# Optimization experiments

Measured on AMD Instinct MI355X. Metric: run time of the kernel, lower is better.

Reference implementation:

```python
import jax, jax.numpy as jnp
import numpy as np

N = 100000   # num_nodes
E = 300000   # num directed edges (symmetrized to 2E inside forward)
D = 128      # input_dim
O = 128      # output_dim
R = 32       # num_relations
B = 8        # num_bases


def setup_inputs() -> dict:
    key = jax.random.key(0)
    ks = jax.random.split(key, 8)
    x = jax.random.normal(ks[0], (N, D), dtype=jnp.float32)
    node_keep_mask = jax.random.randint(ks[1], (N,), 0, 2) > 0
    source = jax.random.randint(ks[2], (E,), 0, N, dtype=jnp.int32)
    target = jax.random.randint(ks[3], (E,), 0, N, dtype=jnp.int32)
    edge_type = jax.random.randint(ks[4], (E,), 0, R, dtype=jnp.int32)
    edge_weights = jax.random.uniform(ks[5], (E,), dtype=jnp.float32)
    # xavier_normal for bases
    std = (2.0 / (D + O)) ** 0.5
    bases = jax.random.normal(ks[6], (B, D, O), dtype=jnp.float32) * std
    # uniform then L1-normalized rows, shape (R+1, B); row R is the self-loop
    rbw = jax.random.uniform(ks[7], (R + 1, B), dtype=jnp.float32)
    rbw = rbw / jnp.sum(rbw, axis=1, keepdims=True)
    return {
        "x": x,
        "node_keep_mask": node_keep_mask,
        "source": source,
        "target": target,
        "edge_type": edge_type,
        "edge_weights": edge_weights,
        "bases": bases,
        "relation_base_weights": rbw,
    }


def reference(x, node_keep_mask, source, target, edge_type, edge_weights,
              bases, relation_base_weights):
    # Self-loop: weight for relation id == num_relations (last row)
    w_self = jnp.einsum("bij,b->ij", bases, relation_base_weights[-1])
    out = jnp.where(node_keep_mask[:, None], x @ w_self, jnp.zeros((), x.dtype))

    # Symmetrize edges: messages flow in both directions (same relation/weight)
    src = jnp.concatenate([source, target])          # (2E,)
    tgt = jnp.concatenate([target, source])          # (2E,)
    etype = jnp.concatenate([edge_type, edge_type])  # (2E,)
    ew = jnp.concatenate([edge_weights, edge_weights])  # (2E,)

    # Project all nodes through every basis once: (N, B, O)
    proj = jnp.einsum("nd,bdo->nbo", x, bases)
    # Per-edge basis coefficients from the edge's relation: (2E, B)
    coeff = relation_base_weights[etype]
    # Message: x[src] @ (sum_b coeff_b * base_b) == sum_b coeff_b * proj[src, b]
    msg = jnp.einsum("eb,ebo->eo", coeff, proj[src])  # (2E, O)
    msg = msg * ew[:, None]

    # Scatter-add messages into target nodes
    out = out.at[tgt].add(msg)
    return out
```

## Files before the change

### kernel.cpp

```cpp
#include <hip/hip_runtime.h>

typedef __attribute__((ext_vector_type(8))) __bf16 bf16x8;
typedef __attribute__((ext_vector_type(4))) float f32x4;
typedef __attribute__((ext_vector_type(2))) float f32x2;
typedef __attribute__((ext_vector_type(8))) unsigned short ushortx8;

__device__ inline unsigned short f2bf(float f) {
  unsigned int u = __float_as_uint(f);
  unsigned int r = (u + 0x7FFFu + ((u >> 16) & 1u)) >> 16;
  return (unsigned short)r;
}

__global__ __launch_bounds__(256) void prep_kernel(const float* __restrict__ x,
                                                   unsigned short* __restrict__ xb, int total8,
                                                   const float* __restrict__ bases,
                                                   unsigned short* __restrict__ bmt,
                                                   const int* __restrict__ src,
                                                   const int* __restrict__ tgt, int E,
                                                   int* __restrict__ cnt,
                                                   const unsigned char* __restrict__ mask,
                                                   int mbytes, int* __restrict__ flag_out,
                                                   int CB, int TB, int HB) {
  int bid = blockIdx.x;
  if (bid < CB) {
    int id = bid * 256 + threadIdx.x;
    if (id >= total8) return;
    f32x4 f0 = ((const f32x4*)x)[2 * id];
    f32x4 f1 = ((const f32x4*)x)[2 * id + 1];
    ushortx8 r;
    r[0] = f2bf(f0[0]); r[1] = f2bf(f0[1]); r[2] = f2bf(f0[2]); r[3] = f2bf(f0[3]);
    r[4] = f2bf(f1[0]); r[5] = f2bf(f1[1]); r[6] = f2bf(f1[2]); r[7] = f2bf(f1[3]);
    ((ushortx8*)xb)[id] = r;
  } else if (bid < CB + TB) {
    int id = (bid - CB) * 256 + threadIdx.x;
    if (id >= 128 * 1024) return;
    int o = id >> 10, k = id & 1023, b = k >> 7, d = k & 127;
    bmt[id] = f2bf(bases[b * 16384 + d * 128 + o]);
  } else if (bid < CB + TB + HB) {
    int i = (bid - CB - TB) * 256 + threadIdx.x;
    if (i >= E) return;
    atomicAdd(&cnt[tgt[i]], 1);
    atomicAdd(&cnt[src[i]], 1);
  } else {
    __shared__ int nz_off, big;
    if (threadIdx.x == 0) { nz_off = 0; big = 0; }
    __syncthreads();
    int lnz = 0, lbig = 0;
    for (int i = threadIdx.x; i < mbytes; i += 256) {
      unsigned char v = mask[i];
      if ((i & 3) && v) lnz++;
      if (v > 1) lbig++;
    }
    if (lnz) atomicAdd(&nz_off, lnz);
    if (lbig) atomicAdd(&big, lbig);
    __syncthreads();
    if (threadIdx.x == 0) *flag_out = (nz_off == 0) ? 0 : ((big == 0) ? 1 : 2);
  }
}

__global__ __launch_bounds__(256) void scan1_kernel(const int* __restrict__ cnt, int N,
                                                    int* __restrict__ bsum) {
  __shared__ int s[256];
  int t = threadIdx.x, i = blockIdx.x * 256 + t;
  s[t] = (i < N) ? cnt[i] : 0;
  __syncthreads();
#pragma unroll
  for (int off = 128; off > 0; off >>= 1) {
    if (t < off) s[t] += s[t + off];
    __syncthreads();
  }
  if (t == 0) bsum[blockIdx.x] = s[0];
}

__global__ void scan2_kernel(const int* __restrict__ bsum, int nb,
                             int* __restrict__ bexcl, int* __restrict__ base, int N) {
  __shared__ int s[512];
  int t = threadIdx.x;
  int v = (t < nb) ? bsum[t] : 0;
  s[t] = v;
  __syncthreads();
  for (int off = 1; off < 512; off <<= 1) {
    int x = (t >= off) ? s[t - off] : 0;
    __syncthreads();
    s[t] += x;
    __syncthreads();
  }
  if (t < nb) bexcl[t] = s[t] - v;
  if (t == nb - 1) base[N] = s[t];
}

__global__ __launch_bounds__(256) void scan3_kernel(const int* __restrict__ cnt, int N,
                                                    const int* __restrict__ bexcl,
                                                    int* __restrict__ base,
                                                    int* __restrict__ cursor) {
  __shared__ int s[256];
  int t = threadIdx.x, i = blockIdx.x * 256 + t;
  int c = (i < N) ? cnt[i] : 0;
  s[t] = c;
  __syncthreads();
  for (int off = 1; off < 256; off <<= 1) {
    int x = (t >= off) ? s[t - off] : 0;
    __syncthreads();
    s[t] += x;
    __syncthreads();
  }
  if (i < N) {
    int v = bexcl[blockIdx.x] + s[t] - c;
    base[i] = v;
    cursor[i] = v;
  }
}

__global__ __launch_bounds__(256) void scatter_kernel(const int* __restrict__ src,
                                                      const int* __restrict__ tgt,
                                                      const int* __restrict__ et,
                                                      const float* __restrict__ ew, int E,
                                                      const float* __restrict__ rbw,
                                                      int* __restrict__ cursor,
                                                      unsigned* __restrict__ msrc,
                                                      uint4* __restrict__ mcoef) {
  __shared__ float ctab[264];
  for (int i = threadIdx.x; i < 264; i += 256) ctab[i] = rbw[i];
  __syncthreads();
  int i = blockIdx.x * 256 + threadIdx.x;
  if (i >= E) return;
  int s = src[i], g = tgt[i], r = et[i];
  float w = ew[i];
  uint4 cv;
  {
    const float* c = &ctab[r * 8];
    cv.x = (unsigned)f2bf(w * c[0]) | ((unsigned)f2bf(w * c[1]) << 16);
    cv.y = (unsigned)f2bf(w * c[2]) | ((unsigned)f2bf(w * c[3]) << 16);
    cv.z = (unsigned)f2bf(w * c[4]) | ((unsigned)f2bf(w * c[5]) << 16);
    cv.w = (unsigned)f2bf(w * c[6]) | ((unsigned)f2bf(w * c[7]) << 16);
  }
  int s1 = atomicAdd(&cursor[g], 1);
  msrc[s1] = (unsigned)s;
  mcoef[s1] = cv;
  int s2 = atomicAdd(&cursor[s], 1);
  msrc[s2] = (unsigned)g;
  mcoef[s2] = cv;
}

__global__ void pad_kernel(unsigned* __restrict__ msrc, uint4* __restrict__ mcoef, int M) {
  int t = threadIdx.x;
  if (t < 8) {
    msrc[M + t] = 0u;
    mcoef[M + t] = make_uint4(0u, 0u, 0u, 0u);
  }
}

__global__ __launch_bounds__(512, 4) void gather_kernel(
    const unsigned* __restrict__ xb32, const unsigned short* __restrict__ bmt,
    const int* __restrict__ base, const unsigned* __restrict__ msrc,
    const uint4* __restrict__ mcoef, const float* __restrict__ rbw,
    const void* __restrict__ maskp, const int* __restrict__ flag_p,
    float* __restrict__ out, int N) {
  extern __shared__ char smem[];
  int t = threadIdx.x;
  int wid = t >> 6, l = t & 63;
  int t0 = blockIdx.x * 32;
  int flag = *flag_p;

  for (int j = 0; j < 4; ++j) {
    int tg = __builtin_amdgcn_readfirstlane(t0 + wid * 4 + j);
    int tgc = min(tg, N - 1);
    int beg = __builtin_amdgcn_readfirstlane(base[tgc]);
    int cnt = __builtin_amdgcn_readfirstlane(base[tgc + 1]) - beg;
    if (tg >= N) cnt = 0;
    unsigned xs = xb32[(size_t)tgc * 64 + l];
    int keep;
    if (flag == 0)      keep = ((const int*)maskp)[tgc] != 0;
    else if (flag == 1) keep = ((const unsigned char*)maskp)[tgc] != 0;
    else                keep = ((const float*)maskp)[tgc] != 0.f;
    float ms = (keep && tg < N) ? 1.f : 0.f;
    f32x2 xv0 = {__uint_as_float(xs << 16), __uint_as_float(xs & 0xFFFF0000u)};
    f32x2 z[8];
#pragma unroll
    for (int b = 0; b < 8; ++b) {
      float a = ms * rbw[256 + b];
      z[b] = (f32x2){a, a} * xv0;
    }
    for (int mb = 0; mb < cnt; mb += 8) {
      unsigned rowv[8];
      uint4 cf[8];
#pragma unroll
      for (int s = 0; s < 8; ++s) {
        rowv[s] = msrc[beg + mb + s];
        cf[s] = mcoef[beg + mb + s];
      }
      unsigned xr[8];
#pragma unroll
      for (int s = 0; s < 8; ++s) xr[s] = xb32[(size_t)rowv[s] * 64 + l];
#pragma unroll
      for (int s = 0; s < 8; ++s) {
        unsigned vm = ((mb + s) < cnt) ? 0xFFFFFFFFu : 0u;
        f32x2 xv = {__uint_as_float(xr[s] << 16), __uint_as_float(xr[s] & 0xFFFF0000u)};
        unsigned cw[4] = {cf[s].x & vm, cf[s].y & vm, cf[s].z & vm, cf[s].w & vm};
#pragma unroll
        for (int q = 0; q < 4; ++q) {
          float a0 = __uint_as_float(cw[q] << 16);
          float a1 = __uint_as_float(cw[q] & 0xFFFF0000u);
          z[2 * q] = __builtin_elementwise_fma((f32x2){a0, a0}, xv, z[2 * q]);
          z[2 * q + 1] = __builtin_elementwise_fma((f32x2){a1, a1}, xv, z[2 * q + 1]);
        }
      }
    }
    int row = wid * 4 + j;
#pragma unroll
    for (int b = 0; b < 8; ++b) {
      unsigned pk = (unsigned)f2bf(z[b][0]) | ((unsigned)f2bf(z[b][1]) << 16);
      int byte = row * 2048 + ((b * 256 + l * 4) ^ ((row & 7) << 4));
      *(unsigned*)(smem + byte) = pk;
    }
  }
  __syncthreads();

  int l15 = l & 15, lk8 = (l >> 4) * 8;
  f32x4 acc[2] = {};
  for (int ks = 0; ks < 32; ++ks) {
    int k0 = ks * 32 + lk8;
    bf16x8 a[2], bb;
#pragma unroll
    for (int rt = 0; rt < 2; ++rt) {
      int tr = rt * 16 + l15;
      int byte = tr * 2048 + ((k0 * 2) ^ ((tr & 7) << 4));
      a[rt] = *(const bf16x8*)(smem + byte);
    }
    int col = wid * 16 + l15;
    bb = *(const bf16x8*)(bmt + (size_t)col * 1024 + k0);
#pragma unroll
    for (int rt = 0; rt < 2; ++rt)
      acc[rt] = __builtin_amdgcn_mfma_f32_16x16x32_bf16(a[rt], bb, acc[rt], 0, 0, 0);
  }
#pragma unroll
  for (int rt = 0; rt < 2; ++rt) {
    int rowb = t0 + rt * 16 + (l >> 4) * 4;
    int col = wid * 16 + l15;
#pragma unroll
    for (int i = 0; i < 4; ++i) {
      int row = rowb + i;
      if (row < N) out[(size_t)row * 128 + col] = acc[rt][i];
    }
  }
}

extern "C" void kernel_launch(void* const* d_in, const int* in_sizes, int n_in,
                              void* d_out, int out_size, void* d_ws, size_t ws_size,
                              hipStream_t stream) {
  const float* x = (const float*)d_in[0];
  const void* mask = d_in[1];
  const int* source = (const int*)d_in[2];
  const int* target = (const int*)d_in[3];
  const int* etype = (const int*)d_in[4];
  const float* eweight = (const float*)d_in[5];
  const float* bases = (const float*)d_in[6];
  const float* rbw = (const float*)d_in[7];
  float* out = (float*)d_out;

  const int N = in_sizes[1];
  const int E = in_sizes[2];
  const int M = 2 * E;
  const int NB = (N + 255) / 256;

  char* ws = (char*)d_ws;
  size_t off = 0;
  unsigned short* xb = (unsigned short*)(ws + off); off += (size_t)N * 256;
  unsigned short* bmt = (unsigned short*)(ws + off); off += 128 * 1024 * 2;
  unsigned* msrc = (unsigned*)(ws + off); off += (size_t)(M + 16) * 4;
  uint4* mcoef = (uint4*)(ws + off); off += (size_t)(M + 16) * 16;
  int* base = (int*)(ws + off); off += ((size_t)N + 64) * 4;
  int* cursor = (int*)(ws + off); off += ((size_t)N + 64) * 4;
  int* cnt = (int*)(ws + off); off += ((size_t)N + 64) * 4;
  int* bsum = (int*)(ws + off); off += 2048;
  int* bexcl = (int*)(ws + off); off += 2048;
  int* flag = (int*)(ws + off); off += 256;

  hipMemsetAsync(cnt, 0, (size_t)N * 4, stream);
  int total8 = (N * 128) / 8;
  int CB = (total8 + 255) / 256;
  int TB = (128 * 1024 + 255) / 256;
  int HB = (E + 255) / 256;
  prep_kernel<<<CB + TB + HB + 1, 256, 0, stream>>>(x, xb, total8, bases, bmt,
                                                    source, target, E, cnt,
                                                    (const unsigned char*)mask,
                                                    N < 8192 ? N : 8192, flag, CB, TB, HB);
  scan1_kernel<<<NB, 256, 0, stream>>>(cnt, N, bsum);
  scan2_kernel<<<1, 512, 0, stream>>>(bsum, NB, bexcl, base, N);
  scan3_kernel<<<NB, 256, 0, stream>>>(cnt, N, bexcl, base, cursor);
  scatter_kernel<<<(E + 255) / 256, 256, 0, stream>>>(source, target, etype, eweight, E,
                                                      rbw, cursor, msrc, mcoef);
  pad_kernel<<<1, 64, 0, stream>>>(msrc, mcoef, M);
  int gblk = (N + 31) / 32;
  size_t shmem = 65536;
  gather_kernel<<<gblk, 512, shmem, stream>>>((const unsigned*)xb, bmt, base, msrc, mcoef,
                                              rbw, mask, flag, out, N);
}
```

Measured before the change: 249.9 us.

## Stage block edge lists in LDS and software-pipeline paired node gathers

The gather kernel now copies each block's message-source indices and coefficients into shared memory when they fit (up to MC entries), then processes two target nodes per wave at once. Row loads for the next group of four messages are double-buffered ahead of the FMAs on the current group, so more gather loads are in flight. This aims to hide gather latency and avoid repeated global index loads, at the cost of more LDS (which may reduce occupancy below 4 blocks per CU) and more registers, plus an extra sync.

```diff
diff --git a/kernel.cpp b/kernel.cpp
--- a/kernel.cpp
+++ b/kernel.cpp
@@ -4,6 +4,8 @@
 typedef __attribute__((ext_vector_type(4))) float f32x4;
 typedef __attribute__((ext_vector_type(2))) float f32x2;
 typedef __attribute__((ext_vector_type(8))) unsigned short ushortx8;
+
+#define MC 384
 
 __device__ inline unsigned short f2bf(float f) {
   unsigned int u = __float_as_uint(f);
@@ -150,6 +152,79 @@
   }
 }
 
+template <bool LDSM>
+__device__ __forceinline__ void load_quad(const unsigned* __restrict__ xb32,
+                                          const unsigned* lms,
+                                          const unsigned* __restrict__ gms, int B0,
+                                          int loc, int mb, int cnt, int l,
+                                          unsigned (&xr)[4]) {
+  if (mb < cnt) {
+#pragma unroll
+    for (int s = 0; s < 4; ++s) {
+      int lo = loc + mb + s;
+      unsigned row = LDSM ? lms[lo] : gms[B0 + lo];
+      xr[s] = xb32[(size_t)row * 64 + l];
+    }
+  }
+}
+
+template <bool LDSM>
+__device__ __forceinline__ void fma_quad(const uint4* lmc,
+                                         const uint4* __restrict__ gmc, int B0,
+                                         int loc, int mb, int cnt,
+                                         const unsigned (&xr)[4], f32x2 (&z)[8]) {
+  if (mb < cnt) {
+#pragma unroll
+    for (int s = 0; s < 4; ++s) {
+      int lo = loc + mb + s;
+      uint4 cf = LDSM ? lmc[lo] : gmc[B0 + lo];
+      unsigned vm = ((mb + s) < cnt) ? 0xFFFFFFFFu : 0u;
+      f32x2 xv = {__uint_as_float(xr[s] << 16), __uint_as_float(xr[s] & 0xFFFF0000u)};
+      unsigned c0 = cf.x & vm, c1 = cf.y & vm, c2 = cf.z & vm, c3 = cf.w & vm;
+      float a;
+      a = __uint_as_float(c0 << 16);          z[0] = __builtin_elementwise_fma((f32x2){a, a}, xv, z[0]);
+      a = __uint_as_float(c0 & 0xFFFF0000u);  z[1] = __builtin_elementwise_fma((f32x2){a, a}, xv, z[1]);
+      a = __uint_as_float(c1 << 16);          z[2] = __builtin_elementwise_fma((f32x2){a, a}, xv, z[2]);
+      a = __uint_as_float(c1 & 0xFFFF0000u);  z[3] = __builtin_elementwise_fma((f32x2){a, a}, xv, z[3]);
+      a = __uint_as_float(c2 << 16);          z[4] = __builtin_elementwise_fma((f32x2){a, a}, xv, z[4]);
+      a = __uint_as_float(c2 & 0xFFFF0000u);  z[5] = __builtin_elementwise_fma((f32x2){a, a}, xv, z[5]);
+      a = __uint_as_float(c3 << 16);          z[6] = __builtin_elementwise_fma((f32x2){a, a}, xv, z[6]);
+      a = __uint_as_float(c3 & 0xFFFF0000u);  z[7] = __builtin_elementwise_fma((f32x2){a, a}, xv, z[7]);
+    }
+  }
+}
+
+template <bool LDSM>
+__device__ __forceinline__ void do_pair(const unsigned* __restrict__ xb32,
+                                        const unsigned* lms, const uint4* lmc,
+                                        const unsigned* __restrict__ gms,
+                                        const uint4* __restrict__ gmc, int B0,
+                                        int locA, int cntA, int locB, int cntB, int l,
+                                        f32x2 (&zA)[8], f32x2 (&zB)[8]) {
+  int rounds = (max(cntA, cntB) + 3) >> 2;
+  if (rounds <= 0) return;
+  unsigned xA0[4], xA1[4], xB0[4], xB1[4];
+  load_quad<LDSM>(xb32, lms, gms, B0, locA, 0, cntA, l, xA0);
+  load_quad<LDSM>(xb32, lms, gms, B0, locB, 0, cntB, l, xB0);
+  int r = 0;
+  while (true) {
+    if (r + 1 < rounds) {
+      load_quad<LDSM>(xb32, lms, gms, B0, locA, (r + 1) * 4, cntA, l, xA1);
+      load_quad<LDSM>(xb32, lms, gms, B0, locB, (r + 1) * 4, cntB, l, xB1);
+    }
+    fma_quad<LDSM>(lmc, gmc, B0, locA, r * 4, cntA, xA0, zA);
+    fma_quad<LDSM>(lmc, gmc, B0, locB, r * 4, cntB, xB0, zB);
+    if (++r >= rounds) break;
+    if (r + 1 < rounds) {
+      load_quad<LDSM>(xb32, lms, gms, B0, locA, (r + 1) * 4, cntA, l, xA0);
+      load_quad<LDSM>(xb32, lms, gms, B0, locB, (r + 1) * 4, cntB, l, xB0);
+    }
+    fma_quad<LDSM>(lmc, gmc, B0, locA, r * 4, cntA, xA1, zA);
+    fma_quad<LDSM>(lmc, gmc, B0, locB, r * 4, cntB, xB1, zB);
+    if (++r >= rounds) break;
+  }
+}
+
 __global__ __launch_bounds__(512, 4) void gather_kernel(
     const unsigned* __restrict__ xb32, const unsigned short* __restrict__ bmt,
     const int* __restrict__ base, const unsigned* __restrict__ msrc,
@@ -157,61 +232,75 @@
     const void* __restrict__ maskp, const int* __restrict__ flag_p,
     float* __restrict__ out, int N) {
   extern __shared__ char smem[];
+  unsigned* lms = (unsigned*)(smem + 65536);
+  uint4* lmc = (uint4*)(smem + 65536 + 1536);
+  int* lbase = (int*)(smem + 65536 + 1536 + 6144);
   int t = threadIdx.x;
   int wid = t >> 6, l = t & 63;
   int t0 = blockIdx.x * 32;
   int flag = *flag_p;
 
-  for (int j = 0; j < 4; ++j) {
-    int tg = __builtin_amdgcn_readfirstlane(t0 + wid * 4 + j);
-    int tgc = min(tg, N - 1);
-    int beg = __builtin_amdgcn_readfirstlane(base[tgc]);
-    int cnt = __builtin_amdgcn_readfirstlane(base[tgc + 1]) - beg;
-    if (tg >= N) cnt = 0;
-    unsigned xs = xb32[(size_t)tgc * 64 + l];
-    int keep;
-    if (flag == 0)      keep = ((const int*)maskp)[tgc] != 0;
-    else if (flag == 1) keep = ((const unsigned char*)maskp)[tgc] != 0;
-    else                keep = ((const float*)maskp)[tgc] != 0.f;
-    float ms = (keep && tg < N) ? 1.f : 0.f;
-    f32x2 xv0 = {__uint_as_float(xs << 16), __uint_as_float(xs & 0xFFFF0000u)};
-    f32x2 z[8];
+  if (t < 33) lbase[t] = base[min(t0 + t, N)];
+  int B0 = __builtin_amdgcn_readfirstlane(base[min(t0, N)]);
+  int B1 = __builtin_amdgcn_readfirstlane(base[min(t0 + 32, N)]);
+  int nm = B1 - B0;
+  bool use_lds = (nm <= MC);
+  if (use_lds) {
+    for (int i = t; i < nm; i += 512) {
+      lms[i] = msrc[B0 + i];
+      lmc[i] = mcoef[B0 + i];
+    }
+    if (t < 8 && nm + t < MC) {
+      lms[nm + t] = 0u;
+      lmc[nm + t] = make_uint4(0u, 0u, 0u, 0u);
+    }
+  }
+  __syncthreads();
+
+  for (int p = 0; p < 2; ++p) {
+    int jA = wid * 4 + p * 2, jB = jA + 1;
+    int tgA = t0 + jA, tgB = t0 + jB;
+    int tcA = min(tgA, N - 1), tcB = min(tgB, N - 1);
+    int begA = __builtin_amdgcn_readfirstlane(lbase[jA]);
+    int begB = __builtin_amdgcn_readfirstlane(lbase[jB]);
+    int endB = __builtin_amdgcn_readfirstlane(lbase[jB + 1]);
+    int cntA = (tgA < N) ? (begB - begA) : 0;
+    int cntB = (tgB < N) ? (endB - begB) : 0;
+    int locA = begA - B0, locB = begB - B0;
+    unsigned xsA = xb32[(size_t)tcA * 64 + l];
+    unsigned xsB = xb32[(size_t)tcB * 64 + l];
+    int keepA, keepB;
+    if (flag == 0) {
+      keepA = ((const int*)maskp)[tcA] != 0; keepB = ((const int*)maskp)[tcB] != 0;
+    } else if (flag == 1) {
+      keepA = ((const unsigned char*)maskp)[tcA] != 0; keepB = ((const unsigned char*)maskp)[tcB] != 0;
+    } else {
+      keepA = ((const float*)maskp)[tcA] != 0.f; keepB = ((const float*)maskp)[tcB] != 0.f;
+    }
+    float msA = (keepA && tgA < N) ? 1.f : 0.f;
+    float msB = (keepB && tgB < N) ? 1.f : 0.f;
+    f32x2 zA[8], zB[8];
+    f32x2 xvA = {__uint_as_float(xsA << 16), __uint_as_float(xsA & 0xFFFF0000u)};
+    f32x2 xvB = {__uint_as_float(xsB << 16), __uint_as_float(xsB & 0xFFFF0000u)};
 #pragma unroll
     for (int b = 0; b < 8; ++b) {
-      float a = ms * rbw[256 + b];
-      z[b] = (f32x2){a, a} * xv0;
-    }
-    for (int mb = 0; mb < cnt; mb += 8) {
-      unsigned rowv[8];
-      uint4 cf[8];
-#pragma unroll
-      for (int s = 0; s < 8; ++s) {
-        rowv[s] = msrc[beg + mb + s];
-        cf[s] = mcoef[beg + mb + s];
-      }
-      unsigned xr[8];
-#pragma unroll
-      for (int s = 0; s < 8; ++s) xr[s] = xb32[(size_t)rowv[s] * 64 + l];
-#pragma unroll
-      for (int s = 0; s < 8; ++s) {
-        unsigned vm = ((mb + s) < cnt) ? 0xFFFFFFFFu : 0u;
-        f32x2 xv = {__uint_as_float(xr[s] << 16), __uint_as_float(xr[s] & 0xFFFF0000u)};
-        unsigned cw[4] = {cf[s].x & vm, cf[s].y & vm, cf[s].z & vm, cf[s].w & vm};
-#pragma unroll
-        for (int q = 0; q < 4; ++q) {
-          float a0 = __uint_as_float(cw[q] << 16);
-          float a1 = __uint_as_float(cw[q] & 0xFFFF0000u);
-          z[2 * q] = __builtin_elementwise_fma((f32x2){a0, a0}, xv, z[2 * q]);
-          z[2 * q + 1] = __builtin_elementwise_fma((f32x2){a1, a1}, xv, z[2 * q + 1]);
-        }
-      }
-    }
-    int row = wid * 4 + j;
+      float cb = rbw[256 + b];
+      float aA = msA * cb, aB = msB * cb;
+      zA[b] = (f32x2){aA, aA} * xvA;
+      zB[b] = (f32x2){aB, aB} * xvB;
+    }
+    if (use_lds)
+      do_pair<true>(xb32, lms, lmc, msrc, mcoef, B0, locA, cntA, locB, cntB, l, zA, zB);
+    else
+      do_pair<false>(xb32, lms, lmc, msrc, mcoef, B0, locA, cntA, locB, cntB, l, zA, zB);
 #pragma unroll
     for (int b = 0; b < 8; ++b) {
-      unsigned pk = (unsigned)f2bf(z[b][0]) | ((unsigned)f2bf(z[b][1]) << 16);
-      int byte = row * 2048 + ((b * 256 + l * 4) ^ ((row & 7) << 4));
-      *(unsigned*)(smem + byte) = pk;
+      unsigned pkA = (unsigned)f2bf(zA[b][0]) | ((unsigned)f2bf(zA[b][1]) << 16);
+      unsigned pkB = (unsigned)f2bf(zB[b][0]) | ((unsigned)f2bf(zB[b][1]) << 16);
+      int byA = jA * 2048 + ((b * 256 + l * 4) ^ ((jA & 7) << 4));
+      int byB = jB * 2048 + ((b * 256 + l * 4) ^ ((jB & 7) << 4));
+      *(unsigned*)(smem + byA) = pkA;
+      *(unsigned*)(smem + byB) = pkB;
     }
   }
   __syncthreads();
@@ -292,7 +381,7 @@
                                                       rbw, cursor, msrc, mcoef);
   pad_kernel<<<1, 64, 0, stream>>>(msrc, mcoef, M);
   int gblk = (N + 31) / 32;
-  size_t shmem = 65536;
+  size_t shmem = 65536 + 1536 + 6144 + 136;
   gather_kernel<<<gblk, 512, shmem, stream>>>((const unsigned*)xb, bmt, base, msrc, mcoef,
                                               rbw, mask, flag, out, N);
 }
```

New measurement: 247.4 us. No clear change (-1.0%).

## Stage block CSR edges in LDS, split waves across two nodes, merge scan kernels

Applied to the files above, without the earlier changes.

The gather kernel now copies each block's edge source indices and coefficients into LDS when they fit, with a global fallback otherwise. Each wave is split into two half-waves that process two target nodes at once, each lane loading 64-bit feature chunks. Edge loads use a double-buffered 4-edge pipeline. The three-kernel prefix scan becomes two kernels, and the padding kernel is folded into the scatter kernel, removing launches. The cost is extra LDS per block, which may lower occupancy, plus divergence when the two nodes in a wave have unequal degrees.

```diff
diff --git a/kernel.cpp b/kernel.cpp
--- a/kernel.cpp
+++ b/kernel.cpp
@@ -2,14 +2,18 @@
 
 typedef __attribute__((ext_vector_type(8))) __bf16 bf16x8;
 typedef __attribute__((ext_vector_type(4))) float f32x4;
-typedef __attribute__((ext_vector_type(2))) float f32x2;
 typedef __attribute__((ext_vector_type(8))) unsigned short ushortx8;
+
+#define MC 384
+#define MCP 448
 
 __device__ inline unsigned short f2bf(float f) {
   unsigned int u = __float_as_uint(f);
   unsigned int r = (u + 0x7FFFu + ((u >> 16) & 1u)) >> 16;
   return (unsigned short)r;
 }
+__device__ inline float bflo(unsigned u) { return __uint_as_float(u << 16); }
+__device__ inline float bfhi(unsigned u) { return __uint_as_float(u & 0xFFFF0000u); }
 
 __global__ __launch_bounds__(256) void prep_kernel(const float* __restrict__ x,
                                                    unsigned short* __restrict__ xb, int total8,
@@ -58,7 +62,7 @@
   }
 }
 
-__global__ __launch_bounds__(256) void scan1_kernel(const int* __restrict__ cnt, int N,
+__global__ __launch_bounds__(256) void scanA_kernel(const int* __restrict__ cnt, int N,
                                                     int* __restrict__ bsum) {
   __shared__ int s[256];
   int t = threadIdx.x, i = blockIdx.x * 256 + t;
@@ -72,29 +76,27 @@
   if (t == 0) bsum[blockIdx.x] = s[0];
 }
 
-__global__ void scan2_kernel(const int* __restrict__ bsum, int nb,
-                             int* __restrict__ bexcl, int* __restrict__ base, int N) {
-  __shared__ int s[512];
-  int t = threadIdx.x;
-  int v = (t < nb) ? bsum[t] : 0;
-  s[t] = v;
-  __syncthreads();
-  for (int off = 1; off < 512; off <<= 1) {
-    int x = (t >= off) ? s[t - off] : 0;
-    __syncthreads();
-    s[t] += x;
-    __syncthreads();
-  }
-  if (t < nb) bexcl[t] = s[t] - v;
-  if (t == nb - 1) base[N] = s[t];
-}
-
-__global__ __launch_bounds__(256) void scan3_kernel(const int* __restrict__ cnt, int N,
-                                                    const int* __restrict__ bexcl,
+__global__ __launch_bounds__(256) void scanB_kernel(const int* __restrict__ cnt, int N,
+                                                    const int* __restrict__ bsum, int NB,
                                                     int* __restrict__ base,
                                                     int* __restrict__ cursor) {
   __shared__ int s[256];
-  int t = threadIdx.x, i = blockIdx.x * 256 + t;
+  __shared__ int spref;
+  int t = threadIdx.x, bid = blockIdx.x;
+  int acc = 0;
+  for (int i = t; i < bid; i += 256) acc += bsum[i];
+  s[t] = acc;
+  __syncthreads();
+#pragma unroll
+  for (int off = 128; off > 0; off >>= 1) {
+    if (t < off) s[t] += s[t + off];
+    __syncthreads();
+  }
+  if (t == 0) spref = s[0];
+  __syncthreads();
+  int pref = spref;
+  __syncthreads();
+  int i = bid * 256 + t;
   int c = (i < N) ? cnt[i] : 0;
   s[t] = c;
   __syncthreads();
@@ -105,10 +107,11 @@
     __syncthreads();
   }
   if (i < N) {
-    int v = bexcl[blockIdx.x] + s[t] - c;
+    int v = pref + s[t] - c;
     base[i] = v;
     cursor[i] = v;
   }
+  if (bid == NB - 1 && t == 255) base[N] = pref + s[255];
 }
 
 __global__ __launch_bounds__(256) void scatter_kernel(const int* __restrict__ src,
@@ -122,6 +125,10 @@
   __shared__ float ctab[264];
   for (int i = threadIdx.x; i < 264; i += 256) ctab[i] = rbw[i];
   __syncthreads();
+  if (blockIdx.x == 0 && threadIdx.x < 80) {
+    msrc[2 * E + threadIdx.x] = 0u;
+    mcoef[2 * E + threadIdx.x] = make_uint4(0u, 0u, 0u, 0u);
+  }
   int i = blockIdx.x * 256 + threadIdx.x;
   if (i >= E) return;
   int s = src[i], g = tgt[i], r = et[i];
@@ -142,76 +149,142 @@
   mcoef[s2] = cv;
 }
 
-__global__ void pad_kernel(unsigned* __restrict__ msrc, uint4* __restrict__ mcoef, int M) {
-  int t = threadIdx.x;
-  if (t < 8) {
-    msrc[M + t] = 0u;
-    mcoef[M + t] = make_uint4(0u, 0u, 0u, 0u);
+template <bool LDSM>
+__device__ __forceinline__ void load4(const uint2* __restrict__ xb64,
+                                      const unsigned* lms, const unsigned* __restrict__ gms,
+                                      int B0, int gcap, int locS, int mb, int ll,
+                                      unsigned Nm1, uint2 (&xq)[4]) {
+#pragma unroll
+  for (int s = 0; s < 4; ++s) {
+    int idx = locS + mb + s;
+    unsigned row;
+    if (LDSM) row = lms[min(idx, MCP - 1)];
+    else      row = gms[min(B0 + idx, gcap)];
+    row = min(row & 0xFFFFFu, Nm1);
+    xq[s] = xb64[(size_t)row * 32 + ll];
+  }
+}
+
+template <bool LDSM>
+__device__ __forceinline__ void fma4(const uint4* lmc, const uint4* __restrict__ gmc,
+                                     int B0, int gcap, int locS, int cntS, int mb,
+                                     const uint2 (&xq)[4], f32x4 (&z)[8]) {
+#pragma unroll
+  for (int s = 0; s < 4; ++s) {
+    int idx = locS + mb + s;
+    uint4 cf;
+    if (LDSM) cf = lmc[min(idx, MCP - 1)];
+    else      cf = gmc[min(B0 + idx, gcap)];
+    unsigned vm = ((mb + s) < cntS) ? 0xFFFFFFFFu : 0u;
+    unsigned c0 = cf.x & vm, c1 = cf.y & vm, c2 = cf.z & vm, c3 = cf.w & vm;
+    f32x4 xv = {bflo(xq[s].x), bfhi(xq[s].x), bflo(xq[s].y), bfhi(xq[s].y)};
+    float a;
+    a = bflo(c0); z[0] = __builtin_elementwise_fma((f32x4){a, a, a, a}, xv, z[0]);
+    a = bfhi(c0); z[1] = __builtin_elementwise_fma((f32x4){a, a, a, a}, xv, z[1]);
+    a = bflo(c1); z[2] = __builtin_elementwise_fma((f32x4){a, a, a, a}, xv, z[2]);
+    a = bfhi(c1); z[3] = __builtin_elementwise_fma((f32x4){a, a, a, a}, xv, z[3]);
+    a = bflo(c2); z[4] = __builtin_elementwise_fma((f32x4){a, a, a, a}, xv, z[4]);
+    a = bfhi(c2); z[5] = __builtin_elementwise_fma((f32x4){a, a, a, a}, xv, z[5]);
+    a = bflo(c3); z[6] = __builtin_elementwise_fma((f32x4){a, a, a, a}, xv, z[6]);
+    a = bfhi(c3); z[7] = __builtin_elementwise_fma((f32x4){a, a, a, a}, xv, z[7]);
+  }
+}
+
+template <bool LDSM>
+__device__ __forceinline__ void duo_loop(const uint2* __restrict__ xb64,
+                                         const unsigned* lms, const uint4* lmc,
+                                         const unsigned* __restrict__ gms,
+                                         const uint4* __restrict__ gmc,
+                                         int B0, int gcap, int locS, int cntS, int rmax,
+                                         int ll, unsigned Nm1, f32x4 (&z)[8]) {
+  int rounds = (rmax + 3) >> 2;
+  if (rounds <= 0) return;
+  uint2 xq0[4], xq1[4];
+  load4<LDSM>(xb64, lms, gms, B0, gcap, locS, 0, ll, Nm1, xq0);
+  for (int r = 0; r < rounds; ++r) {
+    if ((r & 1) == 0) {
+      if (r + 1 < rounds) load4<LDSM>(xb64, lms, gms, B0, gcap, locS, (r + 1) * 4, ll, Nm1, xq1);
+      fma4<LDSM>(lmc, gmc, B0, gcap, locS, cntS, r * 4, xq0, z);
+    } else {
+      if (r + 1 < rounds) load4<LDSM>(xb64, lms, gms, B0, gcap, locS, (r + 1) * 4, ll, Nm1, xq0);
+      fma4<LDSM>(lmc, gmc, B0, gcap, locS, cntS, r * 4, xq1, z);
+    }
   }
 }
 
 __global__ __launch_bounds__(512, 4) void gather_kernel(
-    const unsigned* __restrict__ xb32, const unsigned short* __restrict__ bmt,
+    const uint2* __restrict__ xb64, const unsigned short* __restrict__ bmt,
     const int* __restrict__ base, const unsigned* __restrict__ msrc,
     const uint4* __restrict__ mcoef, const float* __restrict__ rbw,
     const void* __restrict__ maskp, const int* __restrict__ flag_p,
-    float* __restrict__ out, int N) {
+    float* __restrict__ out, int N, int gcap) {
   extern __shared__ char smem[];
+  unsigned* lms = (unsigned*)(smem + 65536);
+  uint4* lmc = (uint4*)(smem + 65536 + MCP * 4);
+  int* lbase = (int*)(smem + 65536 + MCP * 4 + MCP * 16);
   int t = threadIdx.x;
   int wid = t >> 6, l = t & 63;
+  int hw = l >> 5, ll = l & 31;
   int t0 = blockIdx.x * 32;
   int flag = *flag_p;
-
-  for (int j = 0; j < 4; ++j) {
-    int tg = __builtin_amdgcn_readfirstlane(t0 + wid * 4 + j);
-    int tgc = min(tg, N - 1);
-    int beg = __builtin_amdgcn_readfirstlane(base[tgc]);
-    int cnt = __builtin_amdgcn_readfirstlane(base[tgc + 1]) - beg;
-    if (tg >= N) cnt = 0;
-    unsigned xs = xb32[(size_t)tgc * 64 + l];
+  unsigned Nm1 = (unsigned)(N - 1);
+
+  if (t < 33) lbase[t] = base[min(t0 + t, N)];
+  int B0 = __builtin_amdgcn_readfirstlane(base[min(t0, N)]);
+  int B1 = __builtin_amdgcn_readfirstlane(base[min(t0 + 32, N)]);
+  int nm = B1 - B0;
+  bool use_lds = (nm <= MC);
+  if (use_lds) {
+    for (int i = t; i < nm; i += 512) {
+      lms[i] = msrc[B0 + i];
+      lmc[i] = mcoef[B0 + i];
+    }
+    int pz = nm + t;
+    if (t < 64 && pz < MCP) {
+      lms[pz] = 0u;
+      lmc[pz] = make_uint4(0u, 0u, 0u, 0u);
+    }
+  }
+  __syncthreads();
+
+  for (int p = 0; p < 2; ++p) {
+    int jA = wid * 4 + p * 2, jB = jA + 1;
+    int tgA = t0 + jA, tgB = t0 + jB;
+    int begA = __builtin_amdgcn_readfirstlane(lbase[jA]);
+    int begB = __builtin_amdgcn_readfirstlane(lbase[jB]);
+    int endB = __builtin_amdgcn_readfirstlane(lbase[jB + 1]);
+    int cntA = (tgA < N) ? (begB - begA) : 0;
+    int cntB = (tgB < N) ? (endB - begB) : 0;
+    int locA = begA - B0, locB = begB - B0;
+    int tgS = hw ? tgB : tgA;
+    int tcS = min(tgS, N - 1);
+    int locS = hw ? locB : locA;
+    int cntS = hw ? cntB : cntA;
+    uint2 xs = xb64[(size_t)tcS * 32 + ll];
     int keep;
-    if (flag == 0)      keep = ((const int*)maskp)[tgc] != 0;
-    else if (flag == 1) keep = ((const unsigned char*)maskp)[tgc] != 0;
-    else                keep = ((const float*)maskp)[tgc] != 0.f;
-    float ms = (keep && tg < N) ? 1.f : 0.f;
-    f32x2 xv0 = {__uint_as_float(xs << 16), __uint_as_float(xs & 0xFFFF0000u)};
-    f32x2 z[8];
+    if (flag == 0)      keep = ((const int*)maskp)[tcS] != 0;
+    else if (flag == 1) keep = ((const unsigned char*)maskp)[tcS] != 0;
+    else                keep = ((const float*)maskp)[tcS] != 0.f;
+    float ms = (keep && tgS < N) ? 1.f : 0.f;
+    f32x4 xv0 = {bflo(xs.x), bfhi(xs.x), bflo(xs.y), bfhi(xs.y)};
+    f32x4 z[8];
 #pragma unroll
     for (int b = 0; b < 8; ++b) {
       float a = ms * rbw[256 + b];
-      z[b] = (f32x2){a, a} * xv0;
-    }
-    for (int mb = 0; mb < cnt; mb += 8) {
-      unsigned rowv[8];
-      uint4 cf[8];
-#pragma unroll
-      for (int s = 0; s < 8; ++s) {
-        rowv[s] = msrc[beg + mb + s];
-        cf[s] = mcoef[beg + mb + s];
-      }
-      unsigned xr[8];
-#pragma unroll
-      for (int s = 0; s < 8; ++s) xr[s] = xb32[(size_t)rowv[s] * 64 + l];
-#pragma unroll
-      for (int s = 0; s < 8; ++s) {
-        unsigned vm = ((mb + s) < cnt) ? 0xFFFFFFFFu : 0u;
-        f32x2 xv = {__uint_as_float(xr[s] << 16), __uint_as_float(xr[s] & 0xFFFF0000u)};
-        unsigned cw[4] = {cf[s].x & vm, cf[s].y & vm, cf[s].z & vm, cf[s].w & vm};
-#pragma unroll
-        for (int q = 0; q < 4; ++q) {
-          float a0 = __uint_as_float(cw[q] << 16);
-          float a1 = __uint_as_float(cw[q] & 0xFFFF0000u);
-          z[2 * q] = __builtin_elementwise_fma((f32x2){a0, a0}, xv, z[2 * q]);
-          z[2 * q + 1] = __builtin_elementwise_fma((f32x2){a1, a1}, xv, z[2 * q + 1]);
-        }
-      }
-    }
-    int row = wid * 4 + j;
+      z[b] = (f32x4){a, a, a, a} * xv0;
+    }
+    int rmax = max(cntA, cntB);
+    if (use_lds)
+      duo_loop<true>(xb64, lms, lmc, msrc, mcoef, B0, gcap, locS, cntS, rmax, ll, Nm1, z);
+    else
+      duo_loop<false>(xb64, lms, lmc, msrc, mcoef, B0, gcap, locS, cntS, rmax, ll, Nm1, z);
+    int rowS = hw ? jB : jA;
 #pragma unroll
     for (int b = 0; b < 8; ++b) {
-      unsigned pk = (unsigned)f2bf(z[b][0]) | ((unsigned)f2bf(z[b][1]) << 16);
-      int byte = row * 2048 + ((b * 256 + l * 4) ^ ((row & 7) << 4));
-      *(unsigned*)(smem + byte) = pk;
+      unsigned d0 = (unsigned)f2bf(z[b][0]) | ((unsigned)f2bf(z[b][1]) << 16);
+      unsigned d1 = (unsigned)f2bf(z[b][2]) | ((unsigned)f2bf(z[b][3]) << 16);
+      int byte = rowS * 2048 + ((b * 256 + ll * 8) ^ ((rowS & 7) << 4));
+      *(uint2*)(smem + byte) = make_uint2(d0, d1);
     }
   }
   __syncthreads();
@@ -267,13 +340,12 @@
   size_t off = 0;
   unsigned short* xb = (unsigned short*)(ws + off); off += (size_t)N * 256;
   unsigned short* bmt = (unsigned short*)(ws + off); off += 128 * 1024 * 2;
-  unsigned* msrc = (unsigned*)(ws + off); off += (size_t)(M + 16) * 4;
-  uint4* mcoef = (uint4*)(ws + off); off += (size_t)(M + 16) * 16;
+  unsigned* msrc = (unsigned*)(ws + off); off += (size_t)(M + 96) * 4;
+  uint4* mcoef = (uint4*)(ws + off); off += (size_t)(M + 96) * 16;
   int* base = (int*)(ws + off); off += ((size_t)N + 64) * 4;
   int* cursor = (int*)(ws + off); off += ((size_t)N + 64) * 4;
   int* cnt = (int*)(ws + off); off += ((size_t)N + 64) * 4;
   int* bsum = (int*)(ws + off); off += 2048;
-  int* bexcl = (int*)(ws + off); off += 2048;
   int* flag = (int*)(ws + off); off += 256;
 
   hipMemsetAsync(cnt, 0, (size_t)N * 4, stream);
@@ -285,14 +357,12 @@
                                                     source, target, E, cnt,
                                                     (const unsigned char*)mask,
                                                     N < 8192 ? N : 8192, flag, CB, TB, HB);
-  scan1_kernel<<<NB, 256, 0, stream>>>(cnt, N, bsum);
-  scan2_kernel<<<1, 512, 0, stream>>>(bsum, NB, bexcl, base, N);
-  scan3_kernel<<<NB, 256, 0, stream>>>(cnt, N, bexcl, base, cursor);
+  scanA_kernel<<<NB, 256, 0, stream>>>(cnt, N, bsum);
+  scanB_kernel<<<NB, 256, 0, stream>>>(cnt, N, bsum, NB, base, cursor);
   scatter_kernel<<<(E + 255) / 256, 256, 0, stream>>>(source, target, etype, eweight, E,
                                                       rbw, cursor, msrc, mcoef);
-  pad_kernel<<<1, 64, 0, stream>>>(msrc, mcoef, M);
   int gblk = (N + 31) / 32;
-  size_t shmem = 65536;
-  gather_kernel<<<gblk, 512, shmem, stream>>>((const unsigned*)xb, bmt, base, msrc, mcoef,
-                                              rbw, mask, flag, out, N);
-}
+  size_t shmem = 65536 + MCP * 4 + MCP * 16 + 136;
+  gather_kernel<<<gblk, 512, shmem, stream>>>((const uint2*)xb, bmt, base, msrc, mcoef,
+                                              rbw, mask, flag, out, N, M + 79);
+}
```

Measured after the change: 236.6 us. -5.3%, faster.
